# Kernel optimization log

Measured on AMD Instinct MI355X. Metric: run time of the kernel, lower is better.

The kernel has to match this reference:

```python
import jax, jax.numpy as jnp
import numpy as np

N_NODES = 100000
N_EDGES = 1600000
IN_DIM, HID_DIM, OUT_DIM = 128, 64, 128


def _glorot(key, shape):
    fan_in, fan_out = shape[1], shape[0]
    lim = jnp.sqrt(6.0 / (fan_in + fan_out)).astype(jnp.float32)
    return jax.random.uniform(key, shape, jnp.float32, -lim, lim)


def setup_inputs() -> dict:
    key = jax.random.key(0)
    ks = jax.random.split(key, 8)
    x = jax.random.normal(ks[0], (N_NODES, IN_DIM), jnp.float32)
    edge_index = jax.random.randint(ks[1], (2, N_EDGES), 0, N_NODES, jnp.int32)
    # SAGEConv params: lin_l (applied to aggregated neighbors, has bias),
    # lin_r (applied to root/self, no bias) -- PyG convention.
    W_l1 = _glorot(ks[2], (HID_DIM, IN_DIM))
    W_r1 = _glorot(ks[3], (HID_DIM, IN_DIM))
    b1 = jnp.zeros((HID_DIM,), jnp.float32)
    W_l2 = _glorot(ks[4], (OUT_DIM, HID_DIM))
    W_r2 = _glorot(ks[5], (OUT_DIM, HID_DIM))
    b2 = jnp.zeros((OUT_DIM,), jnp.float32)
    return {"x": x, "edge_index": edge_index,
            "W_l1": W_l1, "W_r1": W_r1, "b1": b1,
            "W_l2": W_l2, "W_r2": W_r2, "b2": b2}


def _mean_aggregate(x, src, dst, num_nodes):
    # gather source features per edge, scatter-sum at destination, divide by in-degree
    msg = x[src]                                             # [E, d]
    summed = jax.ops.segment_sum(msg, dst, num_segments=num_nodes)   # [N, d]
    deg = jax.ops.segment_sum(jnp.ones_like(dst, jnp.float32), dst,
                              num_segments=num_nodes)        # [N]
    return summed / jnp.maximum(deg, 1.0)[:, None]


def _sage_conv(x, src, dst, W_l, W_r, b, num_nodes):
    aggr = _mean_aggregate(x, src, dst, num_nodes)
    # out = lin_l(mean_j x_j) + lin_r(x_i)
    return aggr @ W_l.T + b + x @ W_r.T


def reference(x, edge_index, W_l1, W_r1, b1, W_l2, W_r2, b2):
    src, dst = edge_index[0], edge_index[1]
    n = x.shape[0]
    h = _sage_conv(x, src, dst, W_l1, W_r1, b1, n)
    h = jax.nn.relu(h)  # dropout is identity in eval mode
    out = _sage_conv(h, src, dst, W_l2, W_r2, b2, n)
    return out
```

## Files before the change

### kernel.cpp

```cpp
#include <hip/hip_runtime.h>

#define TPB 256
#define BK_SH 8
#define NBMAX 512
#define TILE 4096
#define CAP 8192
#define CAPR 16384

typedef unsigned short ushort_t;
typedef unsigned int uint_t;
typedef __attribute__((ext_vector_type(8))) __bf16 bf8v;
typedef __attribute__((ext_vector_type(4))) float f4v;

__device__ inline ushort_t f2bf(float f) {
    uint_t u = __float_as_uint(f);
    return (ushort_t)((u + 0x7FFFu + ((u >> 16) & 1u)) >> 16);
}
__device__ inline uint_t pack2(float a, float b) {
    return (uint_t)f2bf(a) | ((uint_t)f2bf(b) << 16);
}

union u4bf8 {
    uint4 u;
    bf8v b;
};

__device__ inline void addrow(float* acc, uint4 v) {
    acc[0] += __uint_as_float(v.x << 16);
    acc[1] += __uint_as_float(v.x & 0xFFFF0000u);
    acc[2] += __uint_as_float(v.y << 16);
    acc[3] += __uint_as_float(v.y & 0xFFFF0000u);
    acc[4] += __uint_as_float(v.z << 16);
    acc[5] += __uint_as_float(v.z & 0xFFFF0000u);
    acc[6] += __uint_as_float(v.w << 16);
    acc[7] += __uint_as_float(v.w & 0xFFFF0000u);
}

__global__ __launch_bounds__(NBMAX) void init_cursor_kernel(int* __restrict__ bcursor) {
    bcursor[threadIdx.x] = (int)threadIdx.x * CAPR;
}

__global__ __launch_bounds__(TPB) void bin_scatter_kernel(const int* __restrict__ src,
                                                          const int* __restrict__ dst,
                                                          int* __restrict__ bcursor,
                                                          uint_t* __restrict__ recs,
                                                          int E, int NB) {
    __shared__ uint_t rec[TILE];
    __shared__ ushort_t bb[TILE];
    __shared__ int hist[NBMAX];
    __shared__ int start[NBMAX];
    __shared__ int cur[NBMAX];
    __shared__ int gbase[NBMAX];
    __shared__ int ss[TPB];
    const int tid = threadIdx.x;
    const int t0 = blockIdx.x * TILE;
    const int cnt = min(TILE, E - t0);
    for (int i = tid; i < NBMAX; i += TPB) hist[i] = 0;
    __syncthreads();

    int myS[16], myD[16];
#pragma unroll
    for (int j = 0; j < 16; ++j) {
        int e = t0 + j * TPB + tid;
        if (e < E) {
            myS[j] = src[e];
            myD[j] = dst[e];
            atomicAdd(&hist[myD[j] >> BK_SH], 1);
        } else {
            myD[j] = -1;
        }
    }
    __syncthreads();

    int h0 = hist[2 * tid], h1 = hist[2 * tid + 1];
    int sum2 = h0 + h1;
    ss[tid] = sum2;
    __syncthreads();
    for (int off = 1; off < TPB; off <<= 1) {
        int a = (tid >= off) ? ss[tid - off] : 0;
        __syncthreads();
        ss[tid] += a;
        __syncthreads();
    }
    int ex = ss[tid] - sum2;
    start[2 * tid] = ex;
    start[2 * tid + 1] = ex + h0;
    cur[2 * tid] = ex;
    cur[2 * tid + 1] = ex + h0;
    __syncthreads();

#pragma unroll
    for (int j = 0; j < 16; ++j) {
        if (myD[j] >= 0) {
            int b = myD[j] >> BK_SH;
            int p = atomicAdd(&cur[b], 1);
            rec[p] = ((uint_t)myS[j] << BK_SH) | (uint_t)(myD[j] & ((1 << BK_SH) - 1));
            bb[p] = (ushort_t)b;
        }
    }
    __syncthreads();

    for (int b = tid; b < NB; b += TPB) {
        int c = hist[b];
        gbase[b] = c ? atomicAdd(&bcursor[b], c) : 0;
    }
    __syncthreads();

    for (int i = tid; i < cnt; i += TPB) {
        int b = bb[i];
        recs[gbase[b] + (i - start[b])] = rec[i];
    }
}

__global__ __launch_bounds__(TPB) void bucket_build_kernel(const uint_t* __restrict__ recs,
                                                           const int* __restrict__ bcursor,
                                                           int* __restrict__ rs_beg,
                                                           int* __restrict__ rs_end,
                                                           int* __restrict__ perm, int n) {
    __shared__ int nh[TPB];
    __shared__ int ncur[TPB];
    __shared__ int sscan[TPB];
    __shared__ uint_t stage[CAP];
    const int b = blockIdx.x;
    const int tid = threadIdx.x;
    const int gb = b * CAPR;
    const int cnt = bcursor[b] - gb;
    nh[tid] = 0;
    __syncthreads();
    for (int i = tid; i < cnt; i += TPB)
        atomicAdd(&nh[recs[gb + i] & 255], 1);
    __syncthreads();
    int v = nh[tid];
    sscan[tid] = v;
    __syncthreads();
    for (int off = 1; off < TPB; off <<= 1) {
        int a = (tid >= off) ? sscan[tid - off] : 0;
        __syncthreads();
        sscan[tid] += a;
        __syncthreads();
    }
    int ex = sscan[tid] - v;
    int g = (b << BK_SH) + tid;
    if (g < n) {
        rs_beg[g] = gb + ex;
        rs_end[g] = gb + ex + v;
    }
    ncur[tid] = ex;
    __syncthreads();
    if (cnt <= CAP) {
        for (int i = tid; i < cnt; i += TPB) {
            uint_t r = recs[gb + i];
            int p = atomicAdd(&ncur[r & 255], 1);
            stage[p] = r >> BK_SH;
        }
        __syncthreads();
        for (int i = tid; i < cnt; i += TPB)
            perm[gb + i] = (int)stage[i];
    } else {
        for (int i = tid; i < cnt; i += TPB) {
            uint_t r = recs[gb + i];
            int p = atomicAdd(&ncur[r & 255], 1);
            perm[gb + p] = (int)(r >> BK_SH);
        }
    }
}

__global__ __launch_bounds__(TPB) void cvt_w_kernel(const float* __restrict__ Wl1,
                                                    const float* __restrict__ Wr1,
                                                    const float* __restrict__ Wl2,
                                                    const float* __restrict__ Wr2,
                                                    ushort_t* __restrict__ wl1b,
                                                    ushort_t* __restrict__ wr1b,
                                                    ushort_t* __restrict__ wcat) {
    int i = blockIdx.x * TPB + threadIdx.x;
    if (i < 8192) {
        wl1b[i] = f2bf(Wl1[i]);
        wr1b[i] = f2bf(Wr1[i]);
    }
    if (i < 16384) {
        int c = i >> 7, k = i & 127;
        wcat[i] = (k < 64) ? f2bf(Wl2[c * 64 + k]) : f2bf(Wr2[c * 64 + (k - 64)]);
    }
}

__global__ __launch_bounds__(TPB) void dual_lin_kernel(
    const float* __restrict__ xf, const ushort_t* __restrict__ Wl,
    const ushort_t* __restrict__ Wr, ushort_t* __restrict__ y1b,
    float* __restrict__ zf, int n) {
    const int wave = threadIdx.x >> 6;
    const int lane = threadIdx.x & 63;
    const int l16 = lane & 15;
    const int quad = lane >> 4;
    const int node0 = blockIdx.x * 128 + wave * 32;
    const int koff = quad * 8;

    bf8v wl[4][4], wr[4][4];
#pragma unroll
    for (int ct = 0; ct < 4; ++ct)
#pragma unroll
        for (int kt = 0; kt < 4; ++kt) {
            wl[ct][kt] = *(const bf8v*)(Wl + (ct * 16 + l16) * 128 + kt * 32 + koff);
            wr[ct][kt] = *(const bf8v*)(Wr + (ct * 16 + l16) * 128 + kt * 32 + koff);
        }

    f4v accY[2][4], accZ[2][4];
#pragma unroll
    for (int mt = 0; mt < 2; ++mt)
#pragma unroll
        for (int ct = 0; ct < 4; ++ct) {
            accY[mt][ct] = (f4v)(0.0f);
            accZ[mt][ct] = (f4v)(0.0f);
        }

#pragma unroll
    for (int mt = 0; mt < 2; ++mt) {
        int row = node0 + mt * 16 + l16;
        row = min(row, n - 1);
        bf8v a[4];
#pragma unroll
        for (int kt = 0; kt < 4; ++kt) {
            const float* p = xf + (long long)row * 128 + kt * 32 + koff;
            float4 f0 = *(const float4*)(p);
            float4 f1 = *(const float4*)(p + 4);
            u4bf8 cvt;
            cvt.u.x = pack2(f0.x, f0.y);
            cvt.u.y = pack2(f0.z, f0.w);
            cvt.u.z = pack2(f1.x, f1.y);
            cvt.u.w = pack2(f1.z, f1.w);
            a[kt] = cvt.b;
        }
#pragma unroll
        for (int ct = 0; ct < 4; ++ct)
#pragma unroll
            for (int kt = 0; kt < 4; ++kt) {
                accY[mt][ct] = __builtin_amdgcn_mfma_f32_16x16x32_bf16(
                    a[kt], wl[ct][kt], accY[mt][ct], 0, 0, 0);
                accZ[mt][ct] = __builtin_amdgcn_mfma_f32_16x16x32_bf16(
                    a[kt], wr[ct][kt], accZ[mt][ct], 0, 0, 0);
            }
    }

#pragma unroll
    for (int ct = 0; ct < 4; ++ct) {
        const int col = ct * 16 + l16;
#pragma unroll
        for (int mt = 0; mt < 2; ++mt) {
            int rbase = node0 + mt * 16 + quad * 4;
#pragma unroll
            for (int r = 0; r < 4; ++r) {
                int g = rbase + r;
                if (g >= n) continue;
                y1b[(long long)g * 64 + col] = f2bf(accY[mt][ct][r]);
                zf[(long long)g * 64 + col] = accZ[mt][ct][r];
            }
        }
    }
}

__global__ __launch_bounds__(TPB) void out_mfma_kernel(
    const ushort_t* __restrict__ m2b, const ushort_t* __restrict__ hb,
    const ushort_t* __restrict__ Wc, const float* __restrict__ b2,
    float* __restrict__ out, int n) {
    const int wave = threadIdx.x >> 6;
    const int lane = threadIdx.x & 63;
    const int l16 = lane & 15;
    const int quad = lane >> 4;
    const int cb = wave * 32;
    const int node0 = blockIdx.x * 64;
    const int koff = quad * 8;

    bf8v wb[2][4];
#pragma unroll
    for (int ct = 0; ct < 2; ++ct)
#pragma unroll
        for (int kt = 0; kt < 4; ++kt)
            wb[ct][kt] = *(const bf8v*)(Wc + (cb + ct * 16 + l16) * 128 + kt * 32 + koff);

    f4v acc[4][2];
#pragma unroll
    for (int mt = 0; mt < 4; ++mt)
#pragma unroll
        for (int ct = 0; ct < 2; ++ct) acc[mt][ct] = (f4v)(0.0f);

#pragma unroll
    for (int mt = 0; mt < 4; ++mt) {
        int row = node0 + mt * 16 + l16;
        row = min(row, n - 1);
        bf8v a[4];
        a[0] = *(const bf8v*)(m2b + (long long)row * 64 + koff);
        a[1] = *(const bf8v*)(m2b + (long long)row * 64 + 32 + koff);
        a[2] = *(const bf8v*)(hb + (long long)row * 64 + koff);
        a[3] = *(const bf8v*)(hb + (long long)row * 64 + 32 + koff);
#pragma unroll
        for (int ct = 0; ct < 2; ++ct)
#pragma unroll
            for (int kt = 0; kt < 4; ++kt)
                acc[mt][ct] = __builtin_amdgcn_mfma_f32_16x16x32_bf16(
                    a[kt], wb[ct][kt], acc[mt][ct], 0, 0, 0);
    }

#pragma unroll
    for (int ct = 0; ct < 2; ++ct) {
        const int col = cb + ct * 16 + l16;
        const float bv = b2[col];
#pragma unroll
        for (int mt = 0; mt < 4; ++mt) {
            int rbase = node0 + mt * 16 + quad * 4;
#pragma unroll
            for (int r = 0; r < 4; ++r) {
                int g = rbase + r;
                if (g >= n) continue;
                __builtin_nontemporal_store(acc[mt][ct][r] + bv,
                                            &out[(long long)g * 128 + col]);
            }
        }
    }
}

template <int FUSE>
__global__ __launch_bounds__(TPB) void csr_mean8_kernel(
    const ushort_t* __restrict__ feat, const int* __restrict__ rs_beg,
    const int* __restrict__ rs_end, const int* __restrict__ perm,
    const float* __restrict__ zf, const float* __restrict__ bias,
    ushort_t* __restrict__ outb, int n) {
    long long gt = (long long)blockIdx.x * TPB + threadIdx.x;
    int w = (int)(gt >> 3);
    if (w >= n) return;
    const int cl = threadIdx.x & 7;
    const int beg = rs_beg[w], end = rs_end[w];
    float acc[8];
#pragma unroll
    for (int j = 0; j < 8; ++j) acc[j] = 0.0f;
    const uint4* fp = (const uint4*)feat;
    int e = beg;
    for (; e + 8 <= end; e += 8) {
        int s[8];
#pragma unroll
        for (int j = 0; j < 8; ++j) s[j] = perm[e + j];
        uint4 v[8];
#pragma unroll
        for (int j = 0; j < 8; ++j) v[j] = fp[((long long)s[j] << 3) + cl];
#pragma unroll
        for (int j = 0; j < 8; ++j) addrow(acc, v[j]);
    }
    for (; e + 4 <= end; e += 4) {
        int s0 = perm[e];
        int s1 = perm[e + 1];
        int s2 = perm[e + 2];
        int s3 = perm[e + 3];
        uint4 v0 = fp[((long long)s0 << 3) + cl];
        uint4 v1 = fp[((long long)s1 << 3) + cl];
        uint4 v2 = fp[((long long)s2 << 3) + cl];
        uint4 v3 = fp[((long long)s3 << 3) + cl];
        addrow(acc, v0);
        addrow(acc, v1);
        addrow(acc, v2);
        addrow(acc, v3);
    }
    for (; e < end; ++e) {
        int s = perm[e];
        uint4 v = fp[((long long)s << 3) + cl];
        addrow(acc, v);
    }
    float d = (float)(end - beg);
    float inv = d > 0.f ? 1.f / d : 0.f;
    float r[8];
#pragma unroll
    for (int j = 0; j < 8; ++j) r[j] = acc[j] * inv;
    if (FUSE) {
        const float* zp = zf + (long long)w * 64 + cl * 8;
        float4 z0 = *(const float4*)(zp);
        float4 z1 = *(const float4*)(zp + 4);
        const float* bp = bias + cl * 8;
        float4 b0 = *(const float4*)(bp);
        float4 b1v = *(const float4*)(bp + 4);
        r[0] = fmaxf(r[0] + z0.x + b0.x, 0.0f);
        r[1] = fmaxf(r[1] + z0.y + b0.y, 0.0f);
        r[2] = fmaxf(r[2] + z0.z + b0.z, 0.0f);
        r[3] = fmaxf(r[3] + z0.w + b0.w, 0.0f);
        r[4] = fmaxf(r[4] + z1.x + b1v.x, 0.0f);
        r[5] = fmaxf(r[5] + z1.y + b1v.y, 0.0f);
        r[6] = fmaxf(r[6] + z1.z + b1v.z, 0.0f);
        r[7] = fmaxf(r[7] + z1.w + b1v.w, 0.0f);
    }
    uint4 o4;
    o4.x = pack2(r[0], r[1]);
    o4.y = pack2(r[2], r[3]);
    o4.z = pack2(r[4], r[5]);
    o4.w = pack2(r[6], r[7]);
    ((uint4*)(outb + (long long)w * 64))[cl] = o4;
}

extern "C" void kernel_launch(void* const* d_in, const int* in_sizes, int n_in,
                              void* d_out, int out_size, void* d_ws, size_t ws_size,
                              hipStream_t stream) {
    const float* x = (const float*)d_in[0];
    const int* ei = (const int*)d_in[1];
    const float* Wl1 = (const float*)d_in[2];
    const float* Wr1 = (const float*)d_in[3];
    const float* b1 = (const float*)d_in[4];
    const float* Wl2 = (const float*)d_in[5];
    const float* Wr2 = (const float*)d_in[6];
    const float* b2 = (const float*)d_in[7];
    float* out = (float*)d_out;

    const int n = in_sizes[0] / 128;
    const int E = in_sizes[1] / 2;
    const int* src = ei;
    const int* dst = ei + E;
    const int NB = (n + 255) >> BK_SH;

    char* wsb = (char*)d_ws;
    auto A = [](size_t v) { return (v + 63) & ~(size_t)63; };
    int* bcursor = (int*)wsb;                      size_t o = NBMAX;
    int* rs_beg = (int*)wsb + o;                   o += A(n);
    int* rs_end = (int*)wsb + o;                   o += A(n);
    uint_t* recs = (uint_t*)((int*)wsb + o);       o += (size_t)NB * CAPR;
    int* perm = (int*)wsb + o;                     o += (size_t)NB * CAPR;
    ushort_t* wl1b = (ushort_t*)((int*)wsb + o);   o += 4096;
    ushort_t* wr1b = (ushort_t*)((int*)wsb + o);   o += 4096;
    ushort_t* wcat = (ushort_t*)((int*)wsb + o);   o += 8192;
    ushort_t* fb = (ushort_t*)((int*)wsb + o);     o += A((size_t)n * 32);
    ushort_t* hbuf = (ushort_t*)((int*)wsb + o);   o += A((size_t)n * 32);
    float* zf = (float*)wsb + o;
    ushort_t* m2b = (ushort_t*)zf;

    init_cursor_kernel<<<1, NBMAX, 0, stream>>>(bcursor);
    bin_scatter_kernel<<<(E + TILE - 1) / TILE, TPB, 0, stream>>>(src, dst, bcursor, recs, E, NB);
    bucket_build_kernel<<<NB, TPB, 0, stream>>>(recs, bcursor, rs_beg, rs_end, perm, n);

    cvt_w_kernel<<<64, TPB, 0, stream>>>(Wl1, Wr1, Wl2, Wr2, wl1b, wr1b, wcat);

    const int lblocks = (n + 127) / 128;
    const int mblocks = (int)(((long long)n * 8 + TPB - 1) / TPB);
    const int oblocks = (n + 63) / 64;

    dual_lin_kernel<<<lblocks, TPB, 0, stream>>>(x, wl1b, wr1b, fb, zf, n);
    csr_mean8_kernel<1><<<mblocks, TPB, 0, stream>>>(fb, rs_beg, rs_end, perm, zf, b1, hbuf, n);
    csr_mean8_kernel<0><<<mblocks, TPB, 0, stream>>>(hbuf, rs_beg, rs_end, perm, nullptr, nullptr, m2b, n);
    out_mfma_kernel<<<oblocks, TPB, 0, stream>>>(m2b, hbuf, wcat, b2, out, n);
}
```

Measured before the change: 258.7 us.

## Sort each node's edge list by source range and fold cursor init into weight convert

The bucket build now sub-bins each destination node's edges by the high bits of the source index (in chunks of 16384 nodes), so the CSR neighbor lists come out roughly sorted by source. The intent is better cache locality in the later gather kernels that read feature rows through perm. The cursor initialization also moves into the weight-conversion kernel, which removes one launch. The cost is a larger shared-memory histogram, extra per-thread loops and slightly more index arithmetic in the bucket kernel.

```diff
diff --git a/kernel.cpp b/kernel.cpp
--- a/kernel.cpp
+++ b/kernel.cpp
@@ -6,6 +6,8 @@
 #define TILE 4096
 #define CAP 8192
 #define CAPR 16384
+#define TSH 14
+#define NTMAX 8
 
 typedef unsigned short ushort_t;
 typedef unsigned int uint_t;
@@ -34,10 +36,6 @@
     acc[5] += __uint_as_float(v.z & 0xFFFF0000u);
     acc[6] += __uint_as_float(v.w << 16);
     acc[7] += __uint_as_float(v.w & 0xFFFF0000u);
-}
-
-__global__ __launch_bounds__(NBMAX) void init_cursor_kernel(int* __restrict__ bcursor) {
-    bcursor[threadIdx.x] = (int)threadIdx.x * CAPR;
 }
 
 __global__ __launch_bounds__(TPB) void bin_scatter_kernel(const int* __restrict__ src,
@@ -116,41 +114,52 @@
                                                            const int* __restrict__ bcursor,
                                                            int* __restrict__ rs_beg,
                                                            int* __restrict__ rs_end,
-                                                           int* __restrict__ perm, int n) {
-    __shared__ int nh[TPB];
-    __shared__ int ncur[TPB];
-    __shared__ int sscan[TPB];
+                                                           int* __restrict__ perm,
+                                                           int n, int NT) {
+    __shared__ int nh[TPB * NTMAX];
+    __shared__ int ncur[TPB * NTMAX];
+    __shared__ int ss[TPB];
     __shared__ uint_t stage[CAP];
     const int b = blockIdx.x;
     const int tid = threadIdx.x;
     const int gb = b * CAPR;
     const int cnt = bcursor[b] - gb;
-    nh[tid] = 0;
-    __syncthreads();
-    for (int i = tid; i < cnt; i += TPB)
-        atomicAdd(&nh[recs[gb + i] & 255], 1);
-    __syncthreads();
-    int v = nh[tid];
-    sscan[tid] = v;
+    const int B = TPB * NT;
+    for (int i = tid; i < B; i += TPB) nh[i] = 0;
+    __syncthreads();
+    for (int i = tid; i < cnt; i += TPB) {
+        uint_t r = recs[gb + i];
+        int k = (int)(r & 255u) * NT + (((int)(r >> BK_SH)) >> TSH);
+        atomicAdd(&nh[k], 1);
+    }
+    __syncthreads();
+    int v = 0;
+    for (int t = 0; t < NT; ++t) v += nh[tid * NT + t];
+    ss[tid] = v;
     __syncthreads();
     for (int off = 1; off < TPB; off <<= 1) {
-        int a = (tid >= off) ? sscan[tid - off] : 0;
+        int a = (tid >= off) ? ss[tid - off] : 0;
         __syncthreads();
-        sscan[tid] += a;
+        ss[tid] += a;
         __syncthreads();
     }
-    int ex = sscan[tid] - v;
+    int ex = ss[tid] - v;
     int g = (b << BK_SH) + tid;
     if (g < n) {
         rs_beg[g] = gb + ex;
         rs_end[g] = gb + ex + v;
     }
-    ncur[tid] = ex;
+    int run = ex;
+    for (int t = 0; t < NT; ++t) {
+        ncur[tid * NT + t] = run;
+        run += nh[tid * NT + t];
+    }
     __syncthreads();
     if (cnt <= CAP) {
         for (int i = tid; i < cnt; i += TPB) {
             uint_t r = recs[gb + i];
-            int p = atomicAdd(&ncur[r & 255], 1);
+            int k = (int)(r & 255u) * NT + (((int)(r >> BK_SH)) >> TSH);
+            int p = atomicAdd(&ncur[k], 1);
             stage[p] = r >> BK_SH;
         }
         __syncthreads();
@@ -159,7 +168,8 @@
     } else {
         for (int i = tid; i < cnt; i += TPB) {
             uint_t r = recs[gb + i];
-            int p = atomicAdd(&ncur[r & 255], 1);
+            int k = (int)(r & 255u) * NT + (((int)(r >> BK_SH)) >> TSH);
+            int p = atomicAdd(&ncur[k], 1);
             perm[gb + p] = (int)(r >> BK_SH);
         }
     }
@@ -171,8 +181,10 @@
                                                     const float* __restrict__ Wr2,
                                                     ushort_t* __restrict__ wl1b,
                                                     ushort_t* __restrict__ wr1b,
-                                                    ushort_t* __restrict__ wcat) {
+                                                    ushort_t* __restrict__ wcat,
+                                                    int* __restrict__ bcursor) {
     int i = blockIdx.x * TPB + threadIdx.x;
+    if (i < NBMAX) bcursor[i] = i * CAPR;
     if (i < 8192) {
         wl1b[i] = f2bf(Wl1[i]);
         wr1b[i] = f2bf(Wr1[i]);
@@ -409,6 +421,8 @@
     const int* src = ei;
     const int* dst = ei + E;
     const int NB = (n + 255) >> BK_SH;
+    int NT = (n + (1 << TSH) - 1) >> TSH;
+    if (NT > NTMAX) NT = NTMAX;
 
     char* wsb = (char*)d_ws;
     auto A = [](size_t v) { return (v + 63) & ~(size_t)63; };
@@ -425,11 +439,10 @@
     float* zf = (float*)wsb + o;
     ushort_t* m2b = (ushort_t*)zf;
 
-    init_cursor_kernel<<<1, NBMAX, 0, stream>>>(bcursor);
+    cvt_w_kernel<<<64, TPB, 0, stream>>>(Wl1, Wr1, Wl2, Wr2, wl1b, wr1b, wcat, bcursor);
+
     bin_scatter_kernel<<<(E + TILE - 1) / TILE, TPB, 0, stream>>>(src, dst, bcursor, recs, E, NB);
-    bucket_build_kernel<<<NB, TPB, 0, stream>>>(recs, bcursor, rs_beg, rs_end, perm, n);
-
-    cvt_w_kernel<<<64, TPB, 0, stream>>>(Wl1, Wr1, Wl2, Wr2, wl1b, wr1b, wcat);
+    bucket_build_kernel<<<NB, TPB, 0, stream>>>(recs, bcursor, rs_beg, rs_end, perm, n, NT);
 
     const int lblocks = (n + 127) / 128;
     const int mblocks = (int)(((long long)n * 8 + TPB - 1) / TPB);
```

After: 259.5 us. Within noise of the previous version (+0.3%).

## Sort nodes by degree within buckets to balance CSR mean aggregation

Applied to the files above, without the earlier changes.

Bucket build now counting-sorts the 256 nodes of each bucket by in-degree and writes a node permutation, which both mean-aggregation kernels use to pick which node each 8-lane group handles. Nodes with similar degree then share a wavefront, cutting divergence from uneven edge-loop trip counts. Cursor initialization is folded into the weight conversion kernel, removing one launch. The cost is an extra scan in bucket build and an indirect node lookup with scattered output writes.

```diff
diff --git a/kernel.cpp b/kernel.cpp
--- a/kernel.cpp
+++ b/kernel.cpp
@@ -34,10 +34,6 @@
     acc[5] += __uint_as_float(v.z & 0xFFFF0000u);
     acc[6] += __uint_as_float(v.w << 16);
     acc[7] += __uint_as_float(v.w & 0xFFFF0000u);
-}
-
-__global__ __launch_bounds__(NBMAX) void init_cursor_kernel(int* __restrict__ bcursor) {
-    bcursor[threadIdx.x] = (int)threadIdx.x * CAPR;
 }
 
 __global__ __launch_bounds__(TPB) void bin_scatter_kernel(const int* __restrict__ src,
@@ -116,16 +112,21 @@
                                                            const int* __restrict__ bcursor,
                                                            int* __restrict__ rs_beg,
                                                            int* __restrict__ rs_end,
-                                                           int* __restrict__ perm, int n) {
+                                                           int* __restrict__ perm,
+                                                           int* __restrict__ nodeperm,
+                                                           int n) {
     __shared__ int nh[TPB];
     __shared__ int ncur[TPB];
     __shared__ int sscan[TPB];
+    __shared__ int dh[TPB];
+    __shared__ int dcur[TPB];
     __shared__ uint_t stage[CAP];
     const int b = blockIdx.x;
     const int tid = threadIdx.x;
     const int gb = b * CAPR;
     const int cnt = bcursor[b] - gb;
     nh[tid] = 0;
+    dh[tid] = 0;
     __syncthreads();
     for (int i = tid; i < cnt; i += TPB)
         atomicAdd(&nh[recs[gb + i] & 255], 1);
@@ -146,6 +147,8 @@
         rs_end[g] = gb + ex + v;
     }
     ncur[tid] = ex;
+    int key = (g < n) ? min(v, 254) : 255;
+    atomicAdd(&dh[key], 1);
     __syncthreads();
     if (cnt <= CAP) {
         for (int i = tid; i < cnt; i += TPB) {
@@ -163,6 +166,19 @@
             perm[gb + p] = (int)(r >> BK_SH);
         }
     }
+    int dv = dh[tid];
+    sscan[tid] = dv;
+    __syncthreads();
+    for (int off = 1; off < TPB; off <<= 1) {
+        int a = (tid >= off) ? sscan[tid - off] : 0;
+        __syncthreads();
+        sscan[tid] += a;
+        __syncthreads();
+    }
+    dcur[tid] = sscan[tid] - dv;
+    __syncthreads();
+    int rank = atomicAdd(&dcur[key], 1);
+    nodeperm[(b << BK_SH) + rank] = (g < n) ? g : -1;
 }
 
 __global__ __launch_bounds__(TPB) void cvt_w_kernel(const float* __restrict__ Wl1,
@@ -171,8 +187,10 @@
                                                     const float* __restrict__ Wr2,
                                                     ushort_t* __restrict__ wl1b,
                                                     ushort_t* __restrict__ wr1b,
-                                                    ushort_t* __restrict__ wcat) {
+                                                    ushort_t* __restrict__ wcat,
+                                                    int* __restrict__ bcursor) {
     int i = blockIdx.x * TPB + threadIdx.x;
+    if (i < NBMAX) bcursor[i] = i * CAPR;
     if (i < 8192) {
         wl1b[i] = f2bf(Wl1[i]);
         wr1b[i] = f2bf(Wr1[i]);
@@ -321,11 +339,13 @@
 __global__ __launch_bounds__(TPB) void csr_mean8_kernel(
     const ushort_t* __restrict__ feat, const int* __restrict__ rs_beg,
     const int* __restrict__ rs_end, const int* __restrict__ perm,
-    const float* __restrict__ zf, const float* __restrict__ bias,
-    ushort_t* __restrict__ outb, int n) {
+    const int* __restrict__ nodeperm, const float* __restrict__ zf,
+    const float* __restrict__ bias, ushort_t* __restrict__ outb, int nperm) {
     long long gt = (long long)blockIdx.x * TPB + threadIdx.x;
-    int w = (int)(gt >> 3);
-    if (w >= n) return;
+    int idx = (int)(gt >> 3);
+    if (idx >= nperm) return;
+    int w = nodeperm[idx];
+    if (w < 0) return;
     const int cl = threadIdx.x & 7;
     const int beg = rs_beg[w], end = rs_end[w];
     float acc[8];
@@ -409,12 +429,14 @@
     const int* src = ei;
     const int* dst = ei + E;
     const int NB = (n + 255) >> BK_SH;
+    const int nperm = NB << BK_SH;
 
     char* wsb = (char*)d_ws;
     auto A = [](size_t v) { return (v + 63) & ~(size_t)63; };
     int* bcursor = (int*)wsb;                      size_t o = NBMAX;
     int* rs_beg = (int*)wsb + o;                   o += A(n);
     int* rs_end = (int*)wsb + o;                   o += A(n);
+    int* nodeperm = (int*)wsb + o;                 o += A(nperm);
     uint_t* recs = (uint_t*)((int*)wsb + o);       o += (size_t)NB * CAPR;
     int* perm = (int*)wsb + o;                     o += (size_t)NB * CAPR;
     ushort_t* wl1b = (ushort_t*)((int*)wsb + o);   o += 4096;
@@ -425,18 +447,17 @@
     float* zf = (float*)wsb + o;
     ushort_t* m2b = (ushort_t*)zf;
 
-    init_cursor_kernel<<<1, NBMAX, 0, stream>>>(bcursor);
+    cvt_w_kernel<<<64, TPB, 0, stream>>>(Wl1, Wr1, Wl2, Wr2, wl1b, wr1b, wcat, bcursor);
+
     bin_scatter_kernel<<<(E + TILE - 1) / TILE, TPB, 0, stream>>>(src, dst, bcursor, recs, E, NB);
-    bucket_build_kernel<<<NB, TPB, 0, stream>>>(recs, bcursor, rs_beg, rs_end, perm, n);
-
-    cvt_w_kernel<<<64, TPB, 0, stream>>>(Wl1, Wr1, Wl2, Wr2, wl1b, wr1b, wcat);
+    bucket_build_kernel<<<NB, TPB, 0, stream>>>(recs, bcursor, rs_beg, rs_end, perm, nodeperm, n);
 
     const int lblocks = (n + 127) / 128;
-    const int mblocks = (int)(((long long)n * 8 + TPB - 1) / TPB);
+    const int mblocks = (int)(((long long)nperm * 8 + TPB - 1) / TPB);
     const int oblocks = (n + 63) / 64;
 
     dual_lin_kernel<<<lblocks, TPB, 0, stream>>>(x, wl1b, wr1b, fb, zf, n);
-    csr_mean8_kernel<1><<<mblocks, TPB, 0, stream>>>(fb, rs_beg, rs_end, perm, zf, b1, hbuf, n);
-    csr_mean8_kernel<0><<<mblocks, TPB, 0, stream>>>(hbuf, rs_beg, rs_end, perm, nullptr, nullptr, m2b, n);
+    csr_mean8_kernel<1><<<mblocks, TPB, 0, stream>>>(fb, rs_beg, rs_end, perm, nodeperm, zf, b1, hbuf, nperm);
+    csr_mean8_kernel<0><<<mblocks, TPB, 0, stream>>>(hbuf, rs_beg, rs_end, perm, nodeperm, nullptr, nullptr, m2b, nperm);
     out_mfma_kernel<<<oblocks, TPB, 0, stream>>>(m2b, hbuf, wcat, b2, out, n);
 }
```

Result: slower. 275.4 us (+6.5%).

## Merge edge binning with first linear layer and fuse second aggregation into output GEMM

Applied to the files above, without the earlier changes.

Folds the cursor initialisation into the weight-conversion kernel. Launches edge binning and the first dual linear layer as one grid, split by block index, so the two independent stages can overlap on the GPU. Also fuses the second-layer mean aggregation into the output MFMA kernel, staging the aggregated rows in padded shared memory instead of a global buffer. This cuts three launches and a global round trip, but the fat kernel carries the binning shared memory on every block and the fused output kernel gathers with only 64 nodes per block.

```diff
diff --git a/kernel.cpp b/kernel.cpp
--- a/kernel.cpp
+++ b/kernel.cpp
@@ -6,6 +6,7 @@
 #define TILE 4096
 #define CAP 8192
 #define CAPR 16384
+#define M2LD 72
 
 typedef unsigned short ushort_t;
 typedef unsigned int uint_t;
@@ -36,79 +37,171 @@
     acc[7] += __uint_as_float(v.w & 0xFFFF0000u);
 }
 
-__global__ __launch_bounds__(NBMAX) void init_cursor_kernel(int* __restrict__ bcursor) {
-    bcursor[threadIdx.x] = (int)threadIdx.x * CAPR;
-}
-
-__global__ __launch_bounds__(TPB) void bin_scatter_kernel(const int* __restrict__ src,
-                                                          const int* __restrict__ dst,
-                                                          int* __restrict__ bcursor,
-                                                          uint_t* __restrict__ recs,
-                                                          int E, int NB) {
-    __shared__ uint_t rec[TILE];
-    __shared__ ushort_t bb[TILE];
-    __shared__ int hist[NBMAX];
-    __shared__ int start[NBMAX];
-    __shared__ int cur[NBMAX];
-    __shared__ int gbase[NBMAX];
-    __shared__ int ss[TPB];
+__global__ __launch_bounds__(TPB) void cvt_w_kernel(const float* __restrict__ Wl1,
+                                                    const float* __restrict__ Wr1,
+                                                    const float* __restrict__ Wl2,
+                                                    const float* __restrict__ Wr2,
+                                                    ushort_t* __restrict__ wl1b,
+                                                    ushort_t* __restrict__ wr1b,
+                                                    ushort_t* __restrict__ wcat,
+                                                    int* __restrict__ bcursor) {
+    int i = blockIdx.x * TPB + threadIdx.x;
+    if (i < NBMAX) bcursor[i] = i * CAPR;
+    if (i < 8192) {
+        wl1b[i] = f2bf(Wl1[i]);
+        wr1b[i] = f2bf(Wr1[i]);
+    }
+    if (i < 16384) {
+        int c = i >> 7, k = i & 127;
+        wcat[i] = (k < 64) ? f2bf(Wl2[c * 64 + k]) : f2bf(Wr2[c * 64 + (k - 64)]);
+    }
+}
+
+struct ScatterSmem {
+    uint_t rec[TILE];
+    ushort_t bb[TILE];
+    int hist[NBMAX];
+    int start[NBMAX];
+    int cur[NBMAX];
+    int gbase[NBMAX];
+    int ss[TPB];
+};
+
+__global__ __launch_bounds__(TPB) void fat_kernel(
+    const int* __restrict__ src, const int* __restrict__ dst,
+    int* __restrict__ bcursor, uint_t* __restrict__ recs, int E, int NB, int SB,
+    const float* __restrict__ xf, const ushort_t* __restrict__ Wl,
+    const ushort_t* __restrict__ Wr, ushort_t* __restrict__ y1b,
+    float* __restrict__ zf, int n) {
+    __shared__ ScatterSmem sm;
     const int tid = threadIdx.x;
-    const int t0 = blockIdx.x * TILE;
-    const int cnt = min(TILE, E - t0);
-    for (int i = tid; i < NBMAX; i += TPB) hist[i] = 0;
-    __syncthreads();
-
-    int myS[16], myD[16];
-#pragma unroll
-    for (int j = 0; j < 16; ++j) {
-        int e = t0 + j * TPB + tid;
-        if (e < E) {
-            myS[j] = src[e];
-            myD[j] = dst[e];
-            atomicAdd(&hist[myD[j] >> BK_SH], 1);
-        } else {
-            myD[j] = -1;
-        }
-    }
-    __syncthreads();
-
-    int h0 = hist[2 * tid], h1 = hist[2 * tid + 1];
-    int sum2 = h0 + h1;
-    ss[tid] = sum2;
-    __syncthreads();
-    for (int off = 1; off < TPB; off <<= 1) {
-        int a = (tid >= off) ? ss[tid - off] : 0;
-        __syncthreads();
-        ss[tid] += a;
-        __syncthreads();
-    }
-    int ex = ss[tid] - sum2;
-    start[2 * tid] = ex;
-    start[2 * tid + 1] = ex + h0;
-    cur[2 * tid] = ex;
-    cur[2 * tid + 1] = ex + h0;
-    __syncthreads();
-
-#pragma unroll
-    for (int j = 0; j < 16; ++j) {
-        if (myD[j] >= 0) {
-            int b = myD[j] >> BK_SH;
-            int p = atomicAdd(&cur[b], 1);
-            rec[p] = ((uint_t)myS[j] << BK_SH) | (uint_t)(myD[j] & ((1 << BK_SH) - 1));
-            bb[p] = (ushort_t)b;
-        }
-    }
-    __syncthreads();
-
-    for (int b = tid; b < NB; b += TPB) {
-        int c = hist[b];
-        gbase[b] = c ? atomicAdd(&bcursor[b], c) : 0;
-    }
-    __syncthreads();
-
-    for (int i = tid; i < cnt; i += TPB) {
-        int b = bb[i];
-        recs[gbase[b] + (i - start[b])] = rec[i];
+    if ((int)blockIdx.x < SB) {
+        const int t0 = blockIdx.x * TILE;
+        const int cnt = min(TILE, E - t0);
+        for (int i = tid; i < NBMAX; i += TPB) sm.hist[i] = 0;
+        __syncthreads();
+
+        int myS[16], myD[16];
+#pragma unroll
+        for (int j = 0; j < 16; ++j) {
+            int e = t0 + j * TPB + tid;
+            if (e < E) {
+                myS[j] = src[e];
+                myD[j] = dst[e];
+                atomicAdd(&sm.hist[myD[j] >> BK_SH], 1);
+            } else {
+                myD[j] = -1;
+            }
+        }
+        __syncthreads();
+
+        int h0 = sm.hist[2 * tid], h1 = sm.hist[2 * tid + 1];
+        int sum2 = h0 + h1;
+        sm.ss[tid] = sum2;
+        __syncthreads();
+        for (int off = 1; off < TPB; off <<= 1) {
+            int a = (tid >= off) ? sm.ss[tid - off] : 0;
+            __syncthreads();
+            sm.ss[tid] += a;
+            __syncthreads();
+        }
+        int ex = sm.ss[tid] - sum2;
+        sm.start[2 * tid] = ex;
+        sm.start[2 * tid + 1] = ex + h0;
+        sm.cur[2 * tid] = ex;
+        sm.cur[2 * tid + 1] = ex + h0;
+        __syncthreads();
+
+#pragma unroll
+        for (int j = 0; j < 16; ++j) {
+            if (myD[j] >= 0) {
+                int b = myD[j] >> BK_SH;
+                int p = atomicAdd(&sm.cur[b], 1);
+                sm.rec[p] = ((uint_t)myS[j] << BK_SH) | (uint_t)(myD[j] & ((1 << BK_SH) - 1));
+                sm.bb[p] = (ushort_t)b;
+            }
+        }
+        __syncthreads();
+
+        for (int b = tid; b < NB; b += TPB) {
+            int c = sm.hist[b];
+            sm.gbase[b] = c ? atomicAdd(&bcursor[b], c) : 0;
+        }
+        __syncthreads();
+
+        for (int i = tid; i < cnt; i += TPB) {
+            int b = sm.bb[i];
+            recs[sm.gbase[b] + (i - sm.start[b])] = sm.rec[i];
+        }
+    } else {
+        const int wave = tid >> 6;
+        const int lane = tid & 63;
+        const int l16 = lane & 15;
+        const int quad = lane >> 4;
+        const int node0 = ((int)blockIdx.x - SB) * 128 + wave * 32;
+        const int koff = quad * 8;
+
+        bf8v wl[4][4], wr[4][4];
+#pragma unroll
+        for (int ct = 0; ct < 4; ++ct)
+#pragma unroll
+            for (int kt = 0; kt < 4; ++kt) {
+                wl[ct][kt] = *(const bf8v*)(Wl + (ct * 16 + l16) * 128 + kt * 32 + koff);
+                wr[ct][kt] = *(const bf8v*)(Wr + (ct * 16 + l16) * 128 + kt * 32 + koff);
+            }
+
+        f4v accY[2][4], accZ[2][4];
+#pragma unroll
+        for (int mt = 0; mt < 2; ++mt)
+#pragma unroll
+            for (int ct = 0; ct < 4; ++ct) {
+                accY[mt][ct] = (f4v)(0.0f);
+                accZ[mt][ct] = (f4v)(0.0f);
+            }
+
+#pragma unroll
+        for (int mt = 0; mt < 2; ++mt) {
+            int row = node0 + mt * 16 + l16;
+            row = min(row, n - 1);
+            bf8v a[4];
+#pragma unroll
+            for (int kt = 0; kt < 4; ++kt) {
+                const float* p = xf + (long long)row * 128 + kt * 32 + koff;
+                float4 f0 = *(const float4*)(p);
+                float4 f1 = *(const float4*)(p + 4);
+                u4bf8 cvt;
+                cvt.u.x = pack2(f0.x, f0.y);
+                cvt.u.y = pack2(f0.z, f0.w);
+                cvt.u.z = pack2(f1.x, f1.y);
+                cvt.u.w = pack2(f1.z, f1.w);
+                a[kt] = cvt.b;
+            }
+#pragma unroll
+            for (int ct = 0; ct < 4; ++ct)
+#pragma unroll
+                for (int kt = 0; kt < 4; ++kt) {
+                    accY[mt][ct] = __builtin_amdgcn_mfma_f32_16x16x32_bf16(
+                        a[kt], wl[ct][kt], accY[mt][ct], 0, 0, 0);
+                    accZ[mt][ct] = __builtin_amdgcn_mfma_f32_16x16x32_bf16(
+                        a[kt], wr[ct][kt], accZ[mt][ct], 0, 0, 0);
+                }
+        }
+
+#pragma unroll
+        for (int ct = 0; ct < 4; ++ct) {
+            const int col = ct * 16 + l16;
+#pragma unroll
+            for (int mt = 0; mt < 2; ++mt) {
+                int rbase = node0 + mt * 16 + quad * 4;
+#pragma unroll
+                for (int r = 0; r < 4; ++r) {
+                    int g = rbase + r;
+                    if (g >= n) continue;
+                    y1b[(long long)g * 64 + col] = f2bf(accY[mt][ct][r]);
+                    zf[(long long)g * 64 + col] = accZ[mt][ct][r];
+                }
+            }
+        }
     }
 }
 
@@ -165,159 +258,6 @@
     }
 }
 
-__global__ __launch_bounds__(TPB) void cvt_w_kernel(const float* __restrict__ Wl1,
-                                                    const float* __restrict__ Wr1,
-                                                    const float* __restrict__ Wl2,
-                                                    const float* __restrict__ Wr2,
-                                                    ushort_t* __restrict__ wl1b,
-                                                    ushort_t* __restrict__ wr1b,
-                                                    ushort_t* __restrict__ wcat) {
-    int i = blockIdx.x * TPB + threadIdx.x;
-    if (i < 8192) {
-        wl1b[i] = f2bf(Wl1[i]);
-        wr1b[i] = f2bf(Wr1[i]);
-    }
-    if (i < 16384) {
-        int c = i >> 7, k = i & 127;
-        wcat[i] = (k < 64) ? f2bf(Wl2[c * 64 + k]) : f2bf(Wr2[c * 64 + (k - 64)]);
-    }
-}
-
-__global__ __launch_bounds__(TPB) void dual_lin_kernel(
-    const float* __restrict__ xf, const ushort_t* __restrict__ Wl,
-    const ushort_t* __restrict__ Wr, ushort_t* __restrict__ y1b,
-    float* __restrict__ zf, int n) {
-    const int wave = threadIdx.x >> 6;
-    const int lane = threadIdx.x & 63;
-    const int l16 = lane & 15;
-    const int quad = lane >> 4;
-    const int node0 = blockIdx.x * 128 + wave * 32;
-    const int koff = quad * 8;
-
-    bf8v wl[4][4], wr[4][4];
-#pragma unroll
-    for (int ct = 0; ct < 4; ++ct)
-#pragma unroll
-        for (int kt = 0; kt < 4; ++kt) {
-            wl[ct][kt] = *(const bf8v*)(Wl + (ct * 16 + l16) * 128 + kt * 32 + koff);
-            wr[ct][kt] = *(const bf8v*)(Wr + (ct * 16 + l16) * 128 + kt * 32 + koff);
-        }
-
-    f4v accY[2][4], accZ[2][4];
-#pragma unroll
-    for (int mt = 0; mt < 2; ++mt)
-#pragma unroll
-        for (int ct = 0; ct < 4; ++ct) {
-            accY[mt][ct] = (f4v)(0.0f);
-            accZ[mt][ct] = (f4v)(0.0f);
-        }
-
-#pragma unroll
-    for (int mt = 0; mt < 2; ++mt) {
-        int row = node0 + mt * 16 + l16;
-        row = min(row, n - 1);
-        bf8v a[4];
-#pragma unroll
-        for (int kt = 0; kt < 4; ++kt) {
-            const float* p = xf + (long long)row * 128 + kt * 32 + koff;
-            float4 f0 = *(const float4*)(p);
-            float4 f1 = *(const float4*)(p + 4);
-            u4bf8 cvt;
-            cvt.u.x = pack2(f0.x, f0.y);
-            cvt.u.y = pack2(f0.z, f0.w);
-            cvt.u.z = pack2(f1.x, f1.y);
-            cvt.u.w = pack2(f1.z, f1.w);
-            a[kt] = cvt.b;
-        }
-#pragma unroll
-        for (int ct = 0; ct < 4; ++ct)
-#pragma unroll
-            for (int kt = 0; kt < 4; ++kt) {
-                accY[mt][ct] = __builtin_amdgcn_mfma_f32_16x16x32_bf16(
-                    a[kt], wl[ct][kt], accY[mt][ct], 0, 0, 0);
-                accZ[mt][ct] = __builtin_amdgcn_mfma_f32_16x16x32_bf16(
-                    a[kt], wr[ct][kt], accZ[mt][ct], 0, 0, 0);
-            }
-    }
-
-#pragma unroll
-    for (int ct = 0; ct < 4; ++ct) {
-        const int col = ct * 16 + l16;
-#pragma unroll
-        for (int mt = 0; mt < 2; ++mt) {
-            int rbase = node0 + mt * 16 + quad * 4;
-#pragma unroll
-            for (int r = 0; r < 4; ++r) {
-                int g = rbase + r;
-                if (g >= n) continue;
-                y1b[(long long)g * 64 + col] = f2bf(accY[mt][ct][r]);
-                zf[(long long)g * 64 + col] = accZ[mt][ct][r];
-            }
-        }
-    }
-}
-
-__global__ __launch_bounds__(TPB) void out_mfma_kernel(
-    const ushort_t* __restrict__ m2b, const ushort_t* __restrict__ hb,
-    const ushort_t* __restrict__ Wc, const float* __restrict__ b2,
-    float* __restrict__ out, int n) {
-    const int wave = threadIdx.x >> 6;
-    const int lane = threadIdx.x & 63;
-    const int l16 = lane & 15;
-    const int quad = lane >> 4;
-    const int cb = wave * 32;
-    const int node0 = blockIdx.x * 64;
-    const int koff = quad * 8;
-
-    bf8v wb[2][4];
-#pragma unroll
-    for (int ct = 0; ct < 2; ++ct)
-#pragma unroll
-        for (int kt = 0; kt < 4; ++kt)
-            wb[ct][kt] = *(const bf8v*)(Wc + (cb + ct * 16 + l16) * 128 + kt * 32 + koff);
-
-    f4v acc[4][2];
-#pragma unroll
-    for (int mt = 0; mt < 4; ++mt)
-#pragma unroll
-        for (int ct = 0; ct < 2; ++ct) acc[mt][ct] = (f4v)(0.0f);
-
-#pragma unroll
-    for (int mt = 0; mt < 4; ++mt) {
-        int row = node0 + mt * 16 + l16;
-        row = min(row, n - 1);
-        bf8v a[4];
-        a[0] = *(const bf8v*)(m2b + (long long)row * 64 + koff);
-        a[1] = *(const bf8v*)(m2b + (long long)row * 64 + 32 + koff);
-        a[2] = *(const bf8v*)(hb + (long long)row * 64 + koff);
-        a[3] = *(const bf8v*)(hb + (long long)row * 64 + 32 + koff);
-#pragma unroll
-        for (int ct = 0; ct < 2; ++ct)
-#pragma unroll
-            for (int kt = 0; kt < 4; ++kt)
-                acc[mt][ct] = __builtin_amdgcn_mfma_f32_16x16x32_bf16(
-                    a[kt], wb[ct][kt], acc[mt][ct], 0, 0, 0);
-    }
-
-#pragma unroll
-    for (int ct = 0; ct < 2; ++ct) {
-        const int col = cb + ct * 16 + l16;
-        const float bv = b2[col];
-#pragma unroll
-        for (int mt = 0; mt < 4; ++mt) {
-            int rbase = node0 + mt * 16 + quad * 4;
-#pragma unroll
-            for (int r = 0; r < 4; ++r) {
-                int g = rbase + r;
-                if (g >= n) continue;
-                __builtin_nontemporal_store(acc[mt][ct][r] + bv,
-                                            &out[(long long)g * 128 + col]);
-            }
-        }
-    }
-}
-
-template <int FUSE>
 __global__ __launch_bounds__(TPB) void csr_mean8_kernel(
     const ushort_t* __restrict__ feat, const int* __restrict__ rs_beg,
     const int* __restrict__ rs_end, const int* __restrict__ perm,
@@ -344,10 +284,7 @@
         for (int j = 0; j < 8; ++j) addrow(acc, v[j]);
     }
     for (; e + 4 <= end; e += 4) {
-        int s0 = perm[e];
-        int s1 = perm[e + 1];
-        int s2 = perm[e + 2];
-        int s3 = perm[e + 3];
+        int s0 = perm[e], s1 = perm[e + 1], s2 = perm[e + 2], s3 = perm[e + 3];
         uint4 v0 = fp[((long long)s0 << 3) + cl];
         uint4 v1 = fp[((long long)s1 << 3) + cl];
         uint4 v2 = fp[((long long)s2 << 3) + cl];
@@ -367,28 +304,142 @@
     float r[8];
 #pragma unroll
     for (int j = 0; j < 8; ++j) r[j] = acc[j] * inv;
-    if (FUSE) {
-        const float* zp = zf + (long long)w * 64 + cl * 8;
-        float4 z0 = *(const float4*)(zp);
-        float4 z1 = *(const float4*)(zp + 4);
-        const float* bp = bias + cl * 8;
-        float4 b0 = *(const float4*)(bp);
-        float4 b1v = *(const float4*)(bp + 4);
-        r[0] = fmaxf(r[0] + z0.x + b0.x, 0.0f);
-        r[1] = fmaxf(r[1] + z0.y + b0.y, 0.0f);
-        r[2] = fmaxf(r[2] + z0.z + b0.z, 0.0f);
-        r[3] = fmaxf(r[3] + z0.w + b0.w, 0.0f);
-        r[4] = fmaxf(r[4] + z1.x + b1v.x, 0.0f);
-        r[5] = fmaxf(r[5] + z1.y + b1v.y, 0.0f);
-        r[6] = fmaxf(r[6] + z1.z + b1v.z, 0.0f);
-        r[7] = fmaxf(r[7] + z1.w + b1v.w, 0.0f);
-    }
+    const float* zp = zf + (long long)w * 64 + cl * 8;
+    float4 z0 = *(const float4*)(zp);
+    float4 z1 = *(const float4*)(zp + 4);
+    const float* bp = bias + cl * 8;
+    float4 b0 = *(const float4*)(bp);
+    float4 b1v = *(const float4*)(bp + 4);
+    r[0] = fmaxf(r[0] + z0.x + b0.x, 0.0f);
+    r[1] = fmaxf(r[1] + z0.y + b0.y, 0.0f);
+    r[2] = fmaxf(r[2] + z0.z + b0.z, 0.0f);
+    r[3] = fmaxf(r[3] + z0.w + b0.w, 0.0f);
+    r[4] = fmaxf(r[4] + z1.x + b1v.x, 0.0f);
+    r[5] = fmaxf(r[5] + z1.y + b1v.y, 0.0f);
+    r[6] = fmaxf(r[6] + z1.z + b1v.z, 0.0f);
+    r[7] = fmaxf(r[7] + z1.w + b1v.w, 0.0f);
     uint4 o4;
     o4.x = pack2(r[0], r[1]);
     o4.y = pack2(r[2], r[3]);
     o4.z = pack2(r[4], r[5]);
     o4.w = pack2(r[6], r[7]);
     ((uint4*)(outb + (long long)w * 64))[cl] = o4;
+}
+
+__global__ __launch_bounds__(TPB) void out_fused_kernel(
+    const ushort_t* __restrict__ hb, const int* __restrict__ rs_beg,
+    const int* __restrict__ rs_end, const int* __restrict__ perm,
+    const ushort_t* __restrict__ Wc, const float* __restrict__ b2,
+    float* __restrict__ out, int n) {
+    __shared__ ushort_t m2[64 * M2LD];
+    const int tid = threadIdx.x;
+    const int node0 = blockIdx.x * 64;
+    const int oct = tid >> 3;
+    const int cl = tid & 7;
+    const uint4* fp = (const uint4*)hb;
+
+#pragma unroll
+    for (int half = 0; half < 2; ++half) {
+        int widx = oct + half * 32;
+        int w = node0 + widx;
+        float acc[8];
+#pragma unroll
+        for (int j = 0; j < 8; ++j) acc[j] = 0.0f;
+        float inv = 0.0f;
+        if (w < n) {
+            const int beg = rs_beg[w], end = rs_end[w];
+            int e = beg;
+            for (; e + 8 <= end; e += 8) {
+                int s[8];
+#pragma unroll
+                for (int j = 0; j < 8; ++j) s[j] = perm[e + j];
+                uint4 v[8];
+#pragma unroll
+                for (int j = 0; j < 8; ++j) v[j] = fp[((long long)s[j] << 3) + cl];
+#pragma unroll
+                for (int j = 0; j < 8; ++j) addrow(acc, v[j]);
+            }
+            for (; e + 4 <= end; e += 4) {
+                int s0 = perm[e], s1 = perm[e + 1], s2 = perm[e + 2], s3 = perm[e + 3];
+                uint4 v0 = fp[((long long)s0 << 3) + cl];
+                uint4 v1 = fp[((long long)s1 << 3) + cl];
+                uint4 v2 = fp[((long long)s2 << 3) + cl];
+                uint4 v3 = fp[((long long)s3 << 3) + cl];
+                addrow(acc, v0);
+                addrow(acc, v1);
+                addrow(acc, v2);
+                addrow(acc, v3);
+            }
+            for (; e < end; ++e) {
+                int s = perm[e];
+                uint4 v = fp[((long long)s << 3) + cl];
+                addrow(acc, v);
+            }
+            float d = (float)(end - beg);
+            inv = d > 0.f ? 1.f / d : 0.f;
+        }
+        uint4 o4;
+        o4.x = pack2(acc[0] * inv, acc[1] * inv);
+        o4.y = pack2(acc[2] * inv, acc[3] * inv);
+        o4.z = pack2(acc[4] * inv, acc[5] * inv);
+        o4.w = pack2(acc[6] * inv, acc[7] * inv);
+        *(uint4*)(m2 + widx * M2LD + cl * 8) = o4;
+    }
+    __syncthreads();
+
+    const int wave = tid >> 6;
+    const int lane = tid & 63;
+    const int l16 = lane & 15;
+    const int quad = lane >> 4;
+    const int cb = wave * 32;
+    const int koff = quad * 8;
+
+    bf8v wb[2][4];
+#pragma unroll
+    for (int ct = 0; ct < 2; ++ct)
+#pragma unroll
+        for (int kt = 0; kt < 4; ++kt)
+            wb[ct][kt] = *(const bf8v*)(Wc + (cb + ct * 16 + l16) * 128 + kt * 32 + koff);
+
+    f4v acc2[4][2];
+#pragma unroll
+    for (int mt = 0; mt < 4; ++mt)
+#pragma unroll
+        for (int ct = 0; ct < 2; ++ct) acc2[mt][ct] = (f4v)(0.0f);
+
+#pragma unroll
+    for (int mt = 0; mt < 4; ++mt) {
+        int rl = mt * 16 + l16;
+        int row = min(node0 + rl, n - 1);
+        bf8v a[4];
+        a[0] = *(const bf8v*)(m2 + rl * M2LD + koff);
+        a[1] = *(const bf8v*)(m2 + rl * M2LD + 32 + koff);
+        a[2] = *(const bf8v*)(hb + (long long)row * 64 + koff);
+        a[3] = *(const bf8v*)(hb + (long long)row * 64 + 32 + koff);
+#pragma unroll
+        for (int ct = 0; ct < 2; ++ct)
+#pragma unroll
+            for (int kt = 0; kt < 4; ++kt)
+                acc2[mt][ct] = __builtin_amdgcn_mfma_f32_16x16x32_bf16(
+                    a[kt], wb[ct][kt], acc2[mt][ct], 0, 0, 0);
+    }
+
+#pragma unroll
+    for (int ct = 0; ct < 2; ++ct) {
+        const int col = cb + ct * 16 + l16;
+        const float bv = b2[col];
+#pragma unroll
+        for (int mt = 0; mt < 4; ++mt) {
+            int rbase = node0 + mt * 16 + quad * 4;
+#pragma unroll
+            for (int r = 0; r < 4; ++r) {
+                int g = rbase + r;
+                if (g >= n) continue;
+                __builtin_nontemporal_store(acc2[mt][ct][r] + bv,
+                                            &out[(long long)g * 128 + col]);
+            }
+        }
+    }
 }
 
 extern "C" void kernel_launch(void* const* d_in, const int* in_sizes, int n_in,
@@ -423,20 +474,19 @@
     ushort_t* fb = (ushort_t*)((int*)wsb + o);     o += A((size_t)n * 32);
     ushort_t* hbuf = (ushort_t*)((int*)wsb + o);   o += A((size_t)n * 32);
     float* zf = (float*)wsb + o;
-    ushort_t* m2b = (ushort_t*)zf;
-
-    init_cursor_kernel<<<1, NBMAX, 0, stream>>>(bcursor);
-    bin_scatter_kernel<<<(E + TILE - 1) / TILE, TPB, 0, stream>>>(src, dst, bcursor, recs, E, NB);
+
+    cvt_w_kernel<<<64, TPB, 0, stream>>>(Wl1, Wr1, Wl2, Wr2, wl1b, wr1b, wcat, bcursor);
+
+    const int SB = (E + TILE - 1) / TILE;
+    const int LB = (n + 127) / 128;
+    fat_kernel<<<SB + LB, TPB, 0, stream>>>(src, dst, bcursor, recs, E, NB, SB,
+                                            x, wl1b, wr1b, fb, zf, n);
+
     bucket_build_kernel<<<NB, TPB, 0, stream>>>(recs, bcursor, rs_beg, rs_end, perm, n);
 
-    cvt_w_kernel<<<64, TPB, 0, stream>>>(Wl1, Wr1, Wl2, Wr2, wl1b, wr1b, wcat);
-
-    const int lblocks = (n + 127) / 128;
     const int mblocks = (int)(((long long)n * 8 + TPB - 1) / TPB);
     const int oblocks = (n + 63) / 64;
 
-    dual_lin_kernel<<<lblocks, TPB, 0, stream>>>(x, wl1b, wr1b, fb, zf, n);
-    csr_mean8_kernel<1><<<mblocks, TPB, 0, stream>>>(fb, rs_beg, rs_end, perm, zf, b1, hbuf, n);
-    csr_mean8_kernel<0><<<mblocks, TPB, 0, stream>>>(hbuf, rs_beg, rs_end, perm, nullptr, nullptr, m2b, n);
-    out_mfma_kernel<<<oblocks, TPB, 0, stream>>>(m2b, hbuf, wcat, b2, out, n);
-}
+    csr_mean8_kernel<<<mblocks, TPB, 0, stream>>>(fb, rs_beg, rs_end, perm, zf, b1, hbuf, n);
+    out_fused_kernel<<<oblocks, TPB, 0, stream>>>(hbuf, rs_beg, rs_end, perm, wcat, b2, out, n);
+}
```

Result: faster. 240.6 us (-7.0%).
